# Performance work log

Hardware: AMD Instinct MI355X
Metric: run time of the kernel (lower is better)

Reference implementation:

```python
import jax, jax.numpy as jnp
import numpy as np

L, Q = 256, 21
LAMBDA_H = 1e-06
LAMBDA_J = 0.0001
M = 8192


def setup_inputs() -> dict:
    key = jax.random.key(0)
    k1, k2, k3, k4 = jax.random.split(key, 4)
    seqs = jax.random.randint(k1, (M, L), 0, Q, dtype=jnp.int64 if jax.config.jax_enable_x64 else jnp.int32)
    weights = jax.random.uniform(k2, (M,), dtype=jnp.float32)
    h = jax.random.normal(k3, (L, Q), dtype=jnp.float32) * 0.1
    J = jax.random.normal(k4, (L, L, Q, Q), dtype=jnp.float32) * 0.02
    return {"seqs": seqs, "weights": weights, "h": h, "J": J}


def reference(seqs, weights, h, J):
    # strictly-lower-triangular mask over (i, j): j < i
    tril = jnp.tril(jnp.ones((L, L), dtype=bool), k=-1)
    Jm = J * tril[:, :, None, None]                       # (L, L, q, q)

    # one-hot history; H[b, j, k] = 1 iff seqs[b, j] == k
    H = jax.nn.one_hot(seqs, Q, dtype=h.dtype)            # (M, L, q)

    # contrib[b, i, a] = sum_{j<i, k} J[i, j, a, k] * H[b, j, k]
    # == one big (M, L*q) x (L*q, L*q) causal-masked matmul
    contrib = jnp.einsum('ijak,bjk->bia', Jm, H)          # (M, L, q)

    logits = h[None, :, :] + contrib                      # (M, L, q)
    logp = jax.nn.log_softmax(logits, axis=-1)            # (M, L, q)

    # gather label log-probs
    ll = jnp.take_along_axis(logp, seqs[..., None], axis=-1)[..., 0]  # (M, L)

    M_eff = jnp.maximum(weights.sum(), 1e-12)
    w_norm = weights / M_eff
    nll = -(w_norm[:, None] * ll).sum()

    reg_h = 0.5 * LAMBDA_H * jnp.sum(h ** 2)
    reg_J = 0.5 * LAMBDA_J * jnp.sum(Jm ** 2)
    loss = nll + reg_h + reg_J
    return (loss, nll, reg_h + reg_J)
```

## Files before the change

### kernel.cpp

```cpp
#include <hip/hip_runtime.h>
#include <cstdint>
#include <cstddef>

#define L_   256
#define Q_   21
#define M_   8192
#define QQ   441
#define JCH  16
#define SCALE    32.0f
#define INVSCALE 0.03125f
#define NPAIR ((L_ * (L_ - 1)) / 2)


#define NPREPT 8160
#define GPREP  (NPREPT + 256 + 2)

typedef _Float16 h2 __attribute__((ext_vector_type(2)));
typedef unsigned u32x4 __attribute__((ext_vector_type(4)));

__device__ __forceinline__ float block_reduce_sum(float v) {
    __shared__ float s[256];
    int t = threadIdx.x;
    __syncthreads();
    s[t] = v;
    __syncthreads();
#pragma unroll
    for (int o = 128; o > 0; o >>= 1) {
        if (t < o) s[t] += s[t + o];
        __syncthreads();
    }
    return s[0];
}

__global__ __launch_bounds__(256) void k_prep(const float* __restrict__ J,
                                              const int* __restrict__ seqs,
                                              const float* __restrict__ w,
                                              const float* __restrict__ h,
                                              unsigned* __restrict__ Jt,
                                              unsigned* __restrict__ seqsP,
                                              float* __restrict__ acc2,
                                              float* __restrict__ scal) {
    const int bid = blockIdx.x;
    const int t = threadIdx.x;

    if (bid < NPREPT) {
        __shared__ __align__(16) float sB[4 * 2 * 448];
        const int i  = (bid >> 5) + 1;
        const int j0 = (bid & 31) << 3;
        if (j0 >= i) {
            if (t == 0) acc2[bid] = 0.f;
            return;
        }
        const int jn = min(8, i - j0);
        const int wv = t >> 6;
        const int l  = t & 63;
        const int p0 = wv << 1;
        const int pn = min(2, jn - p0);
        float* sW = sB + wv * (2 * 448);

        float v2 = 0.f;
        for (int pp = 0; pp < pn; ++pp) {
            const float* src = J + (size_t)(i * L_ + j0 + p0 + pp) * QQ;
            float* d = sW + pp * 448;
#pragma unroll
            for (int r = 0; r < 7; ++r) {
                const int idx = (r << 6) + l;
                if (idx < QQ) {
                    float v = __builtin_nontemporal_load(src + idx);
                    d[idx] = v;
                    v2 += v * v;
                }
            }
        }
        __syncthreads();

        const int tri = i * (i - 1) / 2;
        for (int pp = 0; pp < pn; ++pp) {
            const float* s = sW + pp * 448;
            u32x4* dst = reinterpret_cast<u32x4*>(
                Jt + (size_t)(tri + j0 + p0 + pp) * 256);
            unsigned wvv[4];
#pragma unroll
            for (int c = 0; c < 4; ++c) {
                const int dd = (l << 2) | c;
                const int kr = dd / 12;
                const int dw = dd - 12 * kr;
                const int a0 = dw << 1;
                unsigned outw = 0;
                if (kr < Q_) {
                    float x0 = (a0     < Q_) ? s[(a0    ) * Q_ + kr] : 0.f;
                    float x1 = (a0 + 1 < Q_) ? s[(a0 + 1) * Q_ + kr] : 0.f;
                    union { _Float16 hh[2]; unsigned u; } uu;
                    uu.hh[0] = (_Float16)(x0 * SCALE);
                    uu.hh[1] = (_Float16)(x1 * SCALE);
                    outw = uu.u;
                }
                wvv[c] = outw;
            }
            u32x4 o;
            o.x = wvv[0]; o.y = wvv[1]; o.z = wvv[2]; o.w = wvv[3];
            __builtin_nontemporal_store(o, dst + l);
        }

        float r = block_reduce_sum(v2);
        if (t == 0) acc2[bid] = r;
    } else if (bid < NPREPT + 256) {
        const int u  = bid - NPREPT;
        const int b  = ((u >> 3) << 8) + t;
        const int jc = u & 7;
        const int4* row = reinterpret_cast<const int4*>(seqs + (size_t)b * L_);
#pragma unroll
        for (int u8 = 0; u8 < 8; ++u8) {
            const int jq = jc * 8 + u8;
            int4 v = row[jq];
            unsigned p = (unsigned)(v.x & 255) | ((unsigned)(v.y & 255) << 8) |
                         ((unsigned)(v.z & 255) << 16) | ((unsigned)(v.w & 255) << 24);
            seqsP[jq * M_ + b] = p;
        }
    } else if (bid == NPREPT + 256) {
        float v = 0.f;
        for (int x = t; x < M_; x += 256) v += w[x];
        float r = block_reduce_sum(v);
        if (t == 0) scal[0] = r;
    } else {
        float v2 = 0.f;
        for (int x = t; x < L_ * Q_; x += 256) { float y = h[x]; v2 += y * y; }
        float r2 = block_reduce_sum(v2);
        if (t == 0) scal[1] = r2;
    }
}

#define BODY(jj)                                                                    \
    {                                                                               \
        const unsigned kk = (idxw[(jj) >> 2] >> (((jj) & 3) * 8)) & 255u;           \
        const uint4* rp = reinterpret_cast<const uint4*>(sJ) + ((jj) * 64 + kk * 3);\
        union { uint4 u; h2 h[4]; } ra, rb, rc;                                     \
        ra.u = rp[0]; rb.u = rp[1]; rc.u = rp[2];                                   \
        acch[0]  += ra.h[0]; acch[1]  += ra.h[1];                                   \
        acch[2]  += ra.h[2]; acch[3]  += ra.h[3];                                   \
        acch[4]  += rb.h[0]; acch[5]  += rb.h[1];                                   \
        acch[6]  += rb.h[2]; acch[7]  += rb.h[3];                                   \
        acch[8]  += rc.h[0]; acch[9]  += rc.h[1];                                   \
        acch[10] += rc.h[2]; acch[11] += rc.h[3];                                   \
    }

__global__ __launch_bounds__(256, 8) void k_main(const unsigned* __restrict__ Jt,
                                                 const float* __restrict__ h,
                                                 const unsigned* __restrict__ seqsP,
                                                 const float* __restrict__ weights,
                                                 float* __restrict__ accL,
                                                 const int ibase) {
    __shared__ unsigned sJ[JCH * 256];

    const int bid = blockIdx.x;
    const int ii = ((bid >> 5) << 1) | ibase;
    const int i = (L_ - 1) - ii;
    const int b = ((bid & 31) << 8) + threadIdx.x;

    h2 acch[12];
    const float* hp = h + i * Q_;
#pragma unroll
    for (int m = 0; m < 10; ++m) {
        acch[m].x = (_Float16)(hp[2 * m] * SCALE);
        acch[m].y = (_Float16)(hp[2 * m + 1] * SCALE);
    }
    acch[10].x = (_Float16)(hp[20] * SCALE); acch[10].y = (_Float16)0.f;
    acch[11].x = (_Float16)0.f;              acch[11].y = (_Float16)0.f;

    const unsigned* Jrow = Jt + (size_t)(i * (i - 1) / 2) * 256;
    const int nStages = i >> 4;
    const int rem     = i & 15;

    for (int s = 0; s < nStages; ++s) {
        const int j0 = s << 4;
        {
            const uint4* src = reinterpret_cast<const uint4*>(Jrow + j0 * 256);
            uint4* dst = reinterpret_cast<uint4*>(sJ);
#pragma unroll
            for (int n = 0; n < 4; ++n) {
                dst[n * 256 + threadIdx.x] = src[n * 256 + threadIdx.x];
            }
        }
        __syncthreads();

        unsigned idxw[JCH / 4];
#pragma unroll
        for (int q = 0; q < JCH / 4; ++q) {
            idxw[q] = seqsP[((j0 >> 2) + q) * M_ + b];
        }

#pragma unroll
        for (int jj = 0; jj < JCH; ++jj) BODY(jj);

        __syncthreads();
    }

    if (rem) {
        const int j0 = nStages << 4;
        {
            const uint4* src = reinterpret_cast<const uint4*>(Jrow + j0 * 256);
            uint4* dst = reinterpret_cast<uint4*>(sJ);
#pragma unroll
            for (int n = 0; n < 4; ++n) {
                dst[n * 256 + threadIdx.x] = src[n * 256 + threadIdx.x];
            }
        }
        __syncthreads();

        unsigned idxw[JCH / 4];
#pragma unroll
        for (int q = 0; q < JCH / 4; ++q) {
            idxw[q] = seqsP[((j0 >> 2) + q) * M_ + b];
        }

#pragma unroll
        for (int jj = 0; jj < JCH; ++jj) {
            if (jj >= rem) break;
            BODY(jj);
        }
    }

    float l[21];
#pragma unroll
    for (int m = 0; m < 10; ++m) {
        l[2 * m]     = (float)acch[m].x * INVSCALE;
        l[2 * m + 1] = (float)acch[m].y * INVSCALE;
    }
    l[20] = (float)acch[10].x * INVSCALE;

    unsigned lw = seqsP[(i >> 2) * M_ + b];
    int lbl = (int)((lw >> ((i & 3) * 8)) & 255u);

    float m = l[0];
#pragma unroll
    for (int a = 1; a < 21; ++a) m = fmaxf(m, l[a]);
    float s = 0.f;
    float lv = l[0];
#pragma unroll
    for (int a = 0; a < 21; ++a) {
        s += __expf(l[a] - m);
        if (a > 0) lv = (a == lbl) ? l[a] : lv;
    }
    float ll = (lv - m) - __logf(s);
    float contrib = weights[b] * ll;

    float r = block_reduce_sum(contrib);
    if (threadIdx.x == 0) accL[(ibase << 12) + bid] = r;
}

__global__ __launch_bounds__(256) void k_final(const float* __restrict__ acc2,
                                               const float* __restrict__ accL,
                                               const float* __restrict__ scal,
                                               float* __restrict__ out) {
    int t = threadIdx.x;
    float j2 = 0.f;
    for (int x = t; x < NPREPT; x += 256) j2 += acc2[x];
    j2 = block_reduce_sum(j2);
    float lls = 0.f;
    for (int x = t; x < M_; x += 256) lls += accL[x];
    lls = block_reduce_sum(lls);
    if (t == 0) {
        float wsum = fmaxf(scal[0], 1e-12f);
        float nll = -lls / wsum;
        float reg = 0.5e-6f * scal[1] + 0.5e-4f * j2;
        out[0] = nll + reg;
        out[1] = nll;
        out[2] = reg;
    }
}

extern "C" void kernel_launch(void* const* d_in, const int* in_sizes, int n_in,
                              void* d_out, int out_size, void* d_ws, size_t ws_size,
                              hipStream_t stream) {
    const int*   seqs    = (const int*)d_in[0];
    const float* weights = (const float*)d_in[1];
    const float* h       = (const float*)d_in[2];
    const float* J       = (const float*)d_in[3];
    float* out = (float*)d_out;

    char* ws = (char*)d_ws;
    float*    acc2  = (float*)ws;
    float*    accL  = (float*)(ws + 32768);
    float*    scal  = (float*)(ws + 65536);
    unsigned* seqsP = (unsigned*)(ws + 131072);
    unsigned* Jt    = (unsigned*)(ws + 131072 + (size_t)(L_ / 4) * M_ * sizeof(unsigned));


    k_prep<<<GPREP, 256, 0, stream>>>(J, seqs, weights, h, Jt, seqsP, acc2, scal);
    k_main<<<4096, 256, 0, stream>>>(Jt, h, seqsP, weights, accL, 0);
    k_main<<<4096, 256, 0, stream>>>(Jt, h, seqsP, weights, accL, 1);
    k_final<<<1, 256, 0, stream>>>(acc2, accL, scal, out);
}
```

Before: 395.9 us.

## Fuse final reduction into main kernel via atomic ticket and split rows into four launches

Removes the separate single-block final kernel by having each main block atomically add its partial log-likelihood and a last-arriving block (ticket counter) compute the outputs. The main work is split into four launches of 2048 blocks each, with rows interleaved by stride 4, instead of two launches. This adds a memset and global atomics, and trades fewer launch/serialization gaps for more, smaller launches with possibly worse tail balance.

```diff
diff --git a/kernel.cpp b/kernel.cpp
--- a/kernel.cpp
+++ b/kernel.cpp
@@ -148,13 +148,16 @@
                                                  const float* __restrict__ h,
                                                  const unsigned* __restrict__ seqsP,
                                                  const float* __restrict__ weights,
-                                                 float* __restrict__ accL,
-                                                 const int ibase) {
+                                                 const float* __restrict__ acc2,
+                                                 const float* __restrict__ scal,
+                                                 float* __restrict__ lls_total,
+                                                 unsigned* __restrict__ ticket,
+                                                 float* __restrict__ out,
+                                                 const int r4) {
     __shared__ unsigned sJ[JCH * 256];
 
     const int bid = blockIdx.x;
-    const int ii = ((bid >> 5) << 1) | ibase;
-    const int i = (L_ - 1) - ii;
+    const int i = 255 - ((bid >> 5) << 2) - r4;
     const int b = ((bid & 31) << 8) + threadIdx.x;
 
     h2 acch[12];
@@ -245,27 +248,30 @@
     float contrib = weights[b] * ll;
 
     float r = block_reduce_sum(contrib);
-    if (threadIdx.x == 0) accL[(ibase << 12) + bid] = r;
-}
-
-__global__ __launch_bounds__(256) void k_final(const float* __restrict__ acc2,
-                                               const float* __restrict__ accL,
-                                               const float* __restrict__ scal,
-                                               float* __restrict__ out) {
-    int t = threadIdx.x;
-    float j2 = 0.f;
-    for (int x = t; x < NPREPT; x += 256) j2 += acc2[x];
-    j2 = block_reduce_sum(j2);
-    float lls = 0.f;
-    for (int x = t; x < M_; x += 256) lls += accL[x];
-    lls = block_reduce_sum(lls);
-    if (t == 0) {
-        float wsum = fmaxf(scal[0], 1e-12f);
-        float nll = -lls / wsum;
-        float reg = 0.5e-6f * scal[1] + 0.5e-4f * j2;
-        out[0] = nll + reg;
-        out[1] = nll;
-        out[2] = reg;
+
+    __shared__ int win;
+    if (threadIdx.x == 0) {
+        atomicAdd(lls_total, r);
+        __threadfence();
+        unsigned old = atomicAdd(ticket, 1u);
+        win = (old == 8191u) ? 1 : 0;
+    }
+    __syncthreads();
+    if (win) {
+        __threadfence();
+        const int t = threadIdx.x;
+        float j2p = 0.f;
+        for (int x = t; x < NPREPT; x += 256) j2p += acc2[x];
+        float j2 = block_reduce_sum(j2p);
+        if (t == 0) {
+            float lls = atomicAdd(lls_total, 0.0f);
+            float wsum = fmaxf(scal[0], 1e-12f);
+            float nll = -lls / wsum;
+            float reg = 0.5e-6f * scal[1] + 0.5e-4f * j2;
+            out[0] = nll + reg;
+            out[1] = nll;
+            out[2] = reg;
+        }
     }
 }
 
@@ -279,15 +285,18 @@
     float* out = (float*)d_out;
 
     char* ws = (char*)d_ws;
-    float*    acc2  = (float*)ws;
-    float*    accL  = (float*)(ws + 32768);
-    float*    scal  = (float*)(ws + 65536);
-    unsigned* seqsP = (unsigned*)(ws + 131072);
-    unsigned* Jt    = (unsigned*)(ws + 131072 + (size_t)(L_ / 4) * M_ * sizeof(unsigned));
-
+    float*    acc2   = (float*)ws;
+    float*    scal   = (float*)(ws + 65536);
+    float*    llst   = (float*)(ws + 65544);
+    unsigned* ticket = (unsigned*)(ws + 65548);
+    unsigned* seqsP  = (unsigned*)(ws + 131072);
+    unsigned* Jt     = (unsigned*)(ws + 131072 + (size_t)(L_ / 4) * M_ * sizeof(unsigned));
+
+    hipMemsetAsync(ws + 65544, 0, 8, stream);
 
     k_prep<<<GPREP, 256, 0, stream>>>(J, seqs, weights, h, Jt, seqsP, acc2, scal);
-    k_main<<<4096, 256, 0, stream>>>(Jt, h, seqsP, weights, accL, 0);
-    k_main<<<4096, 256, 0, stream>>>(Jt, h, seqsP, weights, accL, 1);
-    k_final<<<1, 256, 0, stream>>>(acc2, accL, scal, out);
+    for (int r = 0; r < 4; ++r) {
+        k_main<<<2048, 256, 0, stream>>>(Jt, h, seqsP, weights, acc2, scal,
+                                         llst, ticket, out, r);
+    }
 }
```

Result: slower. 586.1 us (+48.0%).
